# Kernel tuning notes

Hardware: AMD Instinct MI355X
Metric: run time of the kernel (lower is better)

Reference implementation:

```python
import jax, jax.numpy as jnp
import numpy as np

B, L, C, W, NH, FS = 8, 8, 64, 32, 128, 5
PAD = FS // 2
LN_EPS = 1e-5


def _conv(x, w, b, pad):
    y = jax.lax.conv_general_dilated(x, w, (1, 1), [(pad, pad), (pad, pad)],
                                     dimension_numbers=('NCHW', 'OIHW', 'NCHW'))
    return y + b[None, :, None, None]


def _stem(x, w1, b1, lnw, lnb, w2, b2):
    # conv(fs) -> LayerNorm over [C,W,W] -> ReLU -> conv(1x1)
    y = _conv(x, w1, b1, PAD)
    mu = jnp.mean(y, axis=(1, 2, 3), keepdims=True)
    var = jnp.var(y, axis=(1, 2, 3), keepdims=True)
    y = (y - mu) * jax.lax.rsqrt(var + LN_EPS) * lnw[None] + lnb[None]
    return _conv(jax.nn.relu(y), w2, b2, 0)


def setup_inputs() -> dict:
    key = jax.random.key(0)
    ks = jax.random.split(key, 8)
    f = lambda k, shp: jax.random.normal(k, shp, jnp.float32) * 0.02
    return {
        'in_query': jax.random.normal(ks[0], (B, C, W, W), jnp.float32),
        'in_keys': jax.random.normal(ks[1], (B, L, C, W, W), jnp.float32),
        'in_values': jax.random.normal(ks[2], (B, L, C, W, W), jnp.float32),
        's_w1': f(ks[3], (C, C, FS, FS)), 's_b1': jnp.zeros((C,), jnp.float32),
        's_lnw': jnp.ones((C, W, W), jnp.float32), 's_lnb': jnp.zeros((C, W, W), jnp.float32),
        's_w2': f(ks[4], (NH, C, 1, 1)), 's_b2': jnp.zeros((NH,), jnp.float32),
        'c_w1': f(ks[5], (C, C, FS, FS)), 'c_b1': jnp.zeros((C,), jnp.float32),
        'c_lnw': jnp.ones((C, W, W), jnp.float32), 'c_lnb': jnp.zeros((C, W, W), jnp.float32),
        'c_w2': f(ks[6], (NH, C, 1, 1)), 'c_b2': jnp.zeros((NH,), jnp.float32),
    }


def reference(in_query, in_keys, in_values,
              s_w1, s_b1, s_lnw, s_lnb, s_w2, s_b2,
              c_w1, c_b1, c_lnw, c_lnb, c_w2, c_b2):
    b, c, w, h = in_query.shape
    l = in_keys.shape[1]
    # ---- spatial attention: tokens = pixels, features = channels ----
    qf = in_query.reshape(b, c, w * h).transpose(0, 2, 1)            # [B, WH, C]
    kf = in_keys.transpose(0, 1, 3, 4, 2).reshape(b, l * w * h, c)   # [B, LWH, C]
    vf = in_values.transpose(0, 1, 3, 4, 2).reshape(b, l * w * h, c)
    a_sp = jax.nn.softmax(jnp.einsum('bnc,bmc->bnm', qf, kf), axis=-1)  # [B, WH, LWH]
    sp = jnp.einsum('bnm,bmc->bnc', a_sp, vf).reshape(b, w, h, c).transpose(0, 3, 1, 2)
    # ---- channel attention: tokens = channels, features = pixels ----
    qc = in_query.reshape(b, c, w * h)                               # [B, C, WH]
    kc = in_keys.reshape(b, l * c, h * w)                            # [B, LC, WH]
    vc = in_values.reshape(b, l * c, h * w)
    a_ch = jax.nn.softmax(jnp.einsum('bcn,bmn->bcm', qc, kc), axis=-1)  # [B, C, LC]
    ch = jnp.einsum('bcm,bmn->bcn', a_ch, vc).reshape(b, c, w, h)
    # ---- conv-LN-ReLU-conv stems on residual-added branches ----
    s_attn = _stem(sp + in_query, s_w1, s_b1, s_lnw, s_lnb, s_w2, s_b2)
    c_attn = _stem(ch + in_query, c_w1, c_b1, c_lnw, c_lnb, c_w2, c_b2)
    return (s_attn, c_attn)
```

## Files before the change

kernel.cpp:

```cpp
#include <hip/hip_runtime.h>


#define LOG2E 1.44269504088896340736f

typedef __attribute__((ext_vector_type(8))) short short8;
typedef __attribute__((ext_vector_type(4))) float f4;

#define MFMA16(a, b, c) __builtin_amdgcn_mfma_f32_16x16x32_bf16(a, b, c, 0, 0, 0)

__device__ __forceinline__ unsigned short f2bf(float f) {
  union { float f; unsigned u; } v; v.f = f;
  unsigned r = v.u + 0x7FFFu + ((v.u >> 16) & 1u);
  return (unsigned short)(r >> 16);
}
__device__ __forceinline__ unsigned short f2bf_rz(float f) {
  union { float f; unsigned u; } v; v.f = f;
  return (unsigned short)(v.u >> 16);
}
__device__ __forceinline__ float bf2f(unsigned short h) {
  union { unsigned u; float f; } v; v.u = ((unsigned)h) << 16;
  return v.f;
}
__device__ __forceinline__ float exp2fast(float x) {
#if __has_builtin(__builtin_amdgcn_exp2f)
  return __builtin_amdgcn_exp2f(x);
#else
  return exp2f(x);
#endif
}

#define O_STATS 0ul
#define O_W1T   256ul
#define O_W2B   409856ul
#define O_QT    442624ul
#define O_KSP   1491200ul
#define O_VT    9879808ul
#define O_VCT   18268416ul
#define O_NUM   26657024ul
#define O_DEN   35045632ul
#define O_SP    35307776ul
#define O_PCH   43696384ul
#define O_XS    44220672ul
#define O_XC    45269248ul
#define O_YT    46317824ul

__global__ __launch_bounds__(256) void k1_prep_chanS(
    const float* __restrict__ q, const float* __restrict__ keys,
    const float* __restrict__ values,
    const float* __restrict__ sw1, const float* __restrict__ sw2,
    const float* __restrict__ cw1, const float* __restrict__ cw2,
    char* __restrict__ ws)
{
  __shared__ float T[64][65];
  const int job = blockIdx.x, t = threadIdx.x;

  if (job < 2176) {
    unsigned short* VTp = (unsigned short*)(ws + O_VT);
    unsigned short* KSP = (unsigned short*)(ws + O_KSP);
    unsigned short* VCT = (unsigned short*)(ws + O_VCT);
    unsigned short* QT  = (unsigned short*)(ws + O_QT);
    int kind, mat;
    if (job < 1024)      { kind = 0; mat = job >> 4; }
    else if (job < 2048) { kind = 1; mat = (job - 1024) >> 4; }
    else                 { kind = 2; mat = (job - 2048) >> 4; }
    const int pt = job & 15, p0 = pt * 64;
    const float* src = (kind == 0 ? keys : kind == 1 ? values : q) + (size_t)mat * 65536;

    const int r0 = t >> 4, c4 = (t & 15) * 4;
#pragma unroll
    for (int pass = 0; pass < 4; ++pass) {
      const int r = pass * 16 + r0;
      float4 v = *(const float4*)(src + (size_t)r * 1024 + p0 + c4);
      float vv[4] = {v.x, v.y, v.z, v.w};
      T[r][c4] = vv[0]; T[r][c4 + 1] = vv[1]; T[r][c4 + 2] = vv[2]; T[r][c4 + 3] = vv[3];
      if (kind == 1) {
        int b = mat >> 3, l = mat & 7;
        size_t gi = ((size_t)b * 64 + r) * 8192 + l * 1024 + p0 + c4;
        ushort4 o; unsigned short* op = (unsigned short*)&o;
#pragma unroll
        for (int j = 0; j < 4; ++j) op[j] = f2bf(vv[j]);
        *(ushort4*)(VTp + gi) = o;
      }
    }
    __syncthreads();
#pragma unroll
    for (int pass = 0; pass < 2; ++pass) {
      const int p = pass * 32 + (t >> 3), cs = (t & 7) * 8;
      short8 o;
#pragma unroll
      for (int j = 0; j < 8; ++j) o[j] = (short)f2bf(T[cs + j][p]);
      if (kind == 0) {
        int b = mat >> 3, l = mat & 7;
        *(short8*)(KSP + ((size_t)b * 8192 + l * 1024 + p0 + p) * 64 + cs) = o;
      } else if (kind == 1) {
        int b = mat >> 3, l = mat & 7;
        *(short8*)(VCT + ((size_t)b * 1024 + p0 + p) * 512 + l * 64 + cs) = o;
      } else {
        *(short8*)(QT + ((size_t)mat * 1024 + p0 + p) * 64 + cs) = o;
      }
    }
    return;
  }

  if (job < 3040) {
    unsigned i = (job - 2176) * 256u + t;
    if (i < 204800u) {
      unsigned ci = i & 63u, co = (i >> 6) & 63u, tt = i >> 12;
      unsigned off = tt % 25u, st = tt / 25u;
      const float* w = st ? cw1 : sw1;
      ((unsigned short*)(ws + O_W1T))[i] = f2bf(w[(co * 64u + ci) * 25u + off]);
      return;
    }
    i -= 204800u;
    if (i < 16384u) {
      unsigned c = i & 63u, nh = (i >> 6) & 127u, st = i >> 13;
      const float* w = st ? cw2 : sw2;
      ((unsigned short*)(ws + O_W2B))[i] = f2bf(w[nh * 64u + c]);
    }
    return;
  }

  {
    float* Sp = (float*)(ws + O_SP);
    const int bid = job - 3040;
    const int b = bid >> 6, colT = (bid >> 3) & 7, kt = bid & 7;
    const int w = t >> 6, lane = t & 63;
    const int low4 = lane & 15, quad = lane >> 4;
    const int col0 = colT * 64 + w * 16;

    f4 acc[4];
#pragma unroll
    for (int m = 0; m < 4; ++m) acc[m] = (f4){0.f, 0.f, 0.f, 0.f};

#pragma unroll
    for (int kst = 0; kst < 4; ++kst) {
      const int k = kt * 128 + kst * 32 + quad * 8;
      const float* kp = keys + ((size_t)(b * 512 + col0 + low4)) * 1024 + k;
      float4 u0 = *(const float4*)kp;
      float4 u1 = *(const float4*)(kp + 4);
      float kv[8] = {u0.x, u0.y, u0.z, u0.w, u1.x, u1.y, u1.z, u1.w};
      short8 bh, bl;
#pragma unroll
      for (int j = 0; j < 8; ++j) {
        unsigned short hi = f2bf(kv[j]);
        bh[j] = (short)hi;
        bl[j] = (short)f2bf(kv[j] - bf2f(hi));
      }
#pragma unroll
      for (int m = 0; m < 4; ++m) {
        const float* qp = q + ((size_t)(b * 64 + m * 16 + low4)) * 1024 + k;
        float4 w0 = *(const float4*)qp;
        float4 w1 = *(const float4*)(qp + 4);
        float qv[8] = {w0.x, w0.y, w0.z, w0.w, w1.x, w1.y, w1.z, w1.w};
        short8 ah, al;
#pragma unroll
        for (int j = 0; j < 8; ++j) {
          float sv = qv[j] * LOG2E;
          unsigned short hi = f2bf(sv);
          ah[j] = (short)hi;
          al[j] = (short)f2bf(sv - bf2f(hi));
        }
        acc[m] = MFMA16(ah, bh, acc[m]);
        acc[m] = MFMA16(al, bh, acc[m]);
        acc[m] = MFMA16(ah, bl, acc[m]);
      }
    }
#pragma unroll
    for (int m = 0; m < 4; ++m)
#pragma unroll
      for (int r = 0; r < 4; ++r)
        Sp[(((size_t)kt * 8 + b) * 64 + m * 16 + quad * 4 + r) * 512 + col0 + low4] = acc[m][r];
  }
}

__global__ __launch_bounds__(256) void k2_spat_soft(char* __restrict__ ws)
{
  __shared__ __align__(16) unsigned short Kt[4096];
  __shared__ __align__(16) unsigned short Vt[4096];
  __shared__ __align__(16) unsigned short Plds[4][32][72];

  if (blockIdx.x < 512) {
    const unsigned short* QT = (const unsigned short*)(ws + O_QT);
    const unsigned short* KSP = (const unsigned short*)(ws + O_KSP);
    const unsigned short* VTg = (const unsigned short*)(ws + O_VT);
    unsigned short* NUM = (unsigned short*)(ws + O_NUM);
    float* DEN = (float*)(ws + O_DEN);

    const int b = blockIdx.x >> 6;
    const int qt = (blockIdx.x >> 3) & 7;
    const int s = blockIdx.x & 7;
    const int w = threadIdx.x >> 6, lane = threadIdx.x & 63;
    const int low4 = lane & 15, quad = lane >> 4;

    const unsigned short* KSPb = KSP + (size_t)b * 8192 * 64;
    const unsigned short* VTb = VTg + (size_t)b * 64 * 8192;
    const int qbase = qt * 128 + w * 32;

    short8 qa[2][2];
#pragma unroll
    for (int mi = 0; mi < 2; ++mi)
#pragma unroll
      for (int ks = 0; ks < 2; ++ks) {
        short8 qr = *(const short8*)(QT + ((size_t)(b * 1024 + qbase + mi * 16 + low4)) * 64 + ks * 32 + quad * 8);
        short8 qs;
#pragma unroll
        for (int j = 0; j < 8; ++j) qs[j] = (short)f2bf(bf2f((unsigned short)qr[j]) * LOG2E);
        qa[mi][ks] = qs;
      }

    f4 accO[2][4];
    float den[2][4];
#pragma unroll
    for (int mi = 0; mi < 2; ++mi)
#pragma unroll
      for (int n = 0; n < 4; ++n) {
        accO[mi][n] = (f4){0.f, 0.f, 0.f, 0.f};
        den[mi][n] = 0.f;
      }

    for (int it = 0; it < 16; ++it) {
      const int kv0 = s * 1024 + it * 64;
#pragma unroll
      for (int pass = 0; pass < 2; ++pass) {
        const int id = pass * 256 + threadIdx.x;
        const int n = id >> 7, ks = (id >> 6) & 1, L = (id >> 2) & 15, q = id & 3;
        *(short8*)(&Kt[id * 8]) =
            *(const short8*)(KSPb + (size_t)(kv0 + n * 16 + L) * 64 + ks * 32 + q * 8);
        *(short8*)(&Vt[id * 8]) =
            *(const short8*)(VTb + (size_t)(n * 16 + L) * 8192 + kv0 + ks * 32 + q * 8);
      }
      __syncthreads();

      f4 sS[2][4];
#pragma unroll
      for (int mi = 0; mi < 2; ++mi)
#pragma unroll
        for (int n = 0; n < 4; ++n) sS[mi][n] = (f4){0.f, 0.f, 0.f, 0.f};
#pragma unroll
      for (int ks = 0; ks < 2; ++ks)
#pragma unroll
        for (int n = 0; n < 4; ++n) {
          short8 kb = *(const short8*)(&Kt[((n * 2 + ks) * 64 + low4 * 4 + quad) * 8]);
          sS[0][n] = MFMA16(qa[0][ks], kb, sS[0][n]);
          sS[1][n] = MFMA16(qa[1][ks], kb, sS[1][n]);
        }
#pragma unroll
      for (int mi = 0; mi < 2; ++mi)
#pragma unroll
        for (int n = 0; n < 4; ++n)
#pragma unroll
          for (int r = 0; r < 4; ++r) {
            float e = exp2fast(sS[mi][n][r]);
            den[mi][r] += e;
            Plds[w][mi * 16 + quad * 4 + r][n * 16 + low4] = f2bf_rz(e);
          }
#pragma unroll
      for (int ks = 0; ks < 2; ++ks) {
        short8 pa0 = *(const short8*)&Plds[w][low4][ks * 32 + quad * 8];
        short8 pa1 = *(const short8*)&Plds[w][16 + low4][ks * 32 + quad * 8];
#pragma unroll
        for (int n2 = 0; n2 < 4; ++n2) {
          short8 vb = *(const short8*)(&Vt[((n2 * 2 + ks) * 64 + low4 * 4 + quad) * 8]);
          accO[0][n2] = MFMA16(pa0, vb, accO[0][n2]);
          accO[1][n2] = MFMA16(pa1, vb, accO[1][n2]);
        }
      }
      __syncthreads();
    }

#pragma unroll
    for (int mi = 0; mi < 2; ++mi)
#pragma unroll
      for (int r = 0; r < 4; ++r)
#pragma unroll
        for (int o = 1; o < 16; o <<= 1) den[mi][r] += __shfl_xor(den[mi][r], o, 64);

#pragma unroll
    for (int mi = 0; mi < 2; ++mi)
#pragma unroll
      for (int r = 0; r < 4; ++r) {
        const int row = qbase + mi * 16 + quad * 4 + r;
#pragma unroll
        for (int n2 = 0; n2 < 4; ++n2)
          NUM[(((size_t)(b * 1024 + row)) * 8 + s) * 64 + n2 * 16 + low4] = f2bf(accO[mi][n2][r]);
        if (low4 == 0) DEN[((size_t)(b * 1024 + row)) * 8 + s] = den[mi][r];
      }
    return;
  }

  {
    const float* Sp = (const float*)(ws + O_SP);
    unsigned short* P = (unsigned short*)(ws + O_PCH);
    const int bid = blockIdx.x - 512;
    const int b = bid >> 2, rt = bid & 3;
    const int row = rt * 16 + (threadIdx.x >> 4), tc = threadIdx.x & 15;

    float sv[32];
    float mx = -1e30f;
#pragma unroll
    for (int jj = 0; jj < 32; ++jj) {
      const int col = jj * 16 + tc;
      size_t base = ((size_t)b * 64 + row) * 512 + col;
      float v = 0.f;
#pragma unroll
      for (int kt = 0; kt < 8; ++kt) v += Sp[base + (size_t)kt * 262144];
      sv[jj] = v;
      mx = fmaxf(mx, v);
    }
#pragma unroll
    for (int o = 1; o < 16; o <<= 1) mx = fmaxf(mx, __shfl_xor(mx, o, 64));
    float sum = 0.f;
#pragma unroll
    for (int jj = 0; jj < 32; ++jj) {
      float e = exp2fast(sv[jj] - mx);
      sv[jj] = e;
      sum += e;
    }
#pragma unroll
    for (int o = 1; o < 16; o <<= 1) sum += __shfl_xor(sum, o, 64);
    const float rs = 1.0f / sum;
#pragma unroll
    for (int jj = 0; jj < 32; ++jj)
      P[((size_t)b * 64 + row) * 512 + jj * 16 + tc] = f2bf(sv[jj] * rs);
  }
}

__global__ __launch_bounds__(256) void k3_fin_chanB(char* __restrict__ ws)
{
  const unsigned short* QT = (const unsigned short*)(ws + O_QT);

  if (blockIdx.x < 256) {
    const unsigned short* NUM = (const unsigned short*)(ws + O_NUM);
    const float* DEN = (const float*)(ws + O_DEN);
    unsigned short* Xs = (unsigned short*)(ws + O_XS);

    const unsigned i = blockIdx.x * 256u + threadIdx.x;
    const int c0 = (i & 7) * 8;
    const unsigned row = i >> 3;

    float4 d0 = *(const float4*)(DEN + (size_t)row * 8);
    float4 d1 = *(const float4*)(DEN + (size_t)row * 8 + 4);
    float rd = 1.0f / (d0.x + d0.y + d0.z + d0.w + d1.x + d1.y + d1.z + d1.w);

    float n8[8] = {0, 0, 0, 0, 0, 0, 0, 0};
#pragma unroll
    for (int s = 0; s < 8; ++s) {
      short8 pv = *(const short8*)(NUM + ((size_t)row * 8 + s) * 64 + c0);
#pragma unroll
      for (int j = 0; j < 8; ++j) n8[j] += bf2f((unsigned short)pv[j]);
    }
    size_t ob = (size_t)row * 64 + c0;
    short8 qv = *(const short8*)(QT + ob);
    short8 o8;
#pragma unroll
    for (int j = 0; j < 8; ++j)
      o8[j] = (short)f2bf(n8[j] * rd + bf2f((unsigned short)qv[j]));
    *(short8*)(Xs + ob) = o8;
    return;
  }

  {
    const unsigned short* P = (const unsigned short*)(ws + O_PCH);
    const unsigned short* Vct = (const unsigned short*)(ws + O_VCT);
    unsigned short* Xc = (unsigned short*)(ws + O_XC);

    const int bid = blockIdx.x - 256;
    const int b = bid >> 4, pt = bid & 15;
    const int w = threadIdx.x >> 6, lane = threadIdx.x & 63;
    const int low4 = lane & 15, quad = lane >> 4;
    const int p = pt * 64 + w * 16 + low4;

    f4 acc[4];
#pragma unroll
    for (int m = 0; m < 4; ++m) acc[m] = (f4){0.f, 0.f, 0.f, 0.f};

    for (int ks = 0; ks < 16; ++ks) {
      short8 vb = *(const short8*)(Vct + ((size_t)(b * 1024 + p)) * 512 + ks * 32 + quad * 8);
#pragma unroll
      for (int m = 0; m < 4; ++m) {
        short8 a = *(const short8*)(P + ((size_t)(b * 64 + m * 16 + low4)) * 512 + ks * 32 + quad * 8);
        acc[m] = MFMA16(a, vb, acc[m]);
      }
    }
#pragma unroll
    for (int m = 0; m < 4; ++m)
#pragma unroll
      for (int r = 0; r < 4; ++r) {
        const int c = m * 16 + quad * 4 + r;
        size_t o = ((size_t)(b * 1024 + p)) * 64 + c;
        Xc[o] = f2bf(acc[m][r] + bf2f(QT[o]));
      }
  }
}

__global__ __launch_bounds__(256) void k4_conv5(char* __restrict__ ws,
                                                const float* __restrict__ sb1,
                                                const float* __restrict__ cb1)
{
  const int id = blockIdx.x;
  const int s = id >> 8, b = (id >> 5) & 7, pt = id & 31;
  const int w = threadIdx.x >> 6, lane = threadIdx.x & 63;
  const int low4 = lane & 15, quad = lane >> 4;
  const int wsub = w & 1, half = w >> 1;

  const unsigned short* X = (const unsigned short*)(ws + (s ? O_XC : O_XS));
  const unsigned short* W1t = (const unsigned short*)(ws + O_W1T);
  unsigned short* Yt = (unsigned short*)(ws + O_YT);
  float* stats = (float*)(ws + O_STATS);
  const float* b1p = s ? cb1 : sb1;

  __shared__ float Hbuf[2][16][65];
  __shared__ float red[2][2];

  const int p = pt * 32 + wsub * 16 + low4;
  const int y0 = p >> 5, x0 = p & 31;

  f4 acc[4];
#pragma unroll
  for (int m = 0; m < 4; ++m) acc[m] = (f4){0.f, 0.f, 0.f, 0.f};

  const int o0 = half ? 13 : 0, o1 = half ? 25 : 13;
  for (int off = o0; off < o1; ++off) {
    const int dy = off / 5 - 2, dx = off % 5 - 2;
    const int ys = y0 + dy, xs = x0 + dx;
    const bool valid = ((unsigned)ys < 32u) & ((unsigned)xs < 32u);
    const int psrc = valid ? (p + dy * 32 + dx) : p;
    const unsigned short* xp = X + ((size_t)(b * 1024 + psrc)) * 64;
    const unsigned short* wp = W1t + ((size_t)((s * 25 + off) * 64)) * 64;
#pragma unroll
    for (int ks = 0; ks < 2; ++ks) {
      short8 bv = *(const short8*)(xp + ks * 32 + quad * 8);
      if (!valid) bv = (short8)0;
#pragma unroll
      for (int m = 0; m < 4; ++m) {
        short8 av = *(const short8*)(wp + (m * 16 + low4) * 64 + ks * 32 + quad * 8);
        acc[m] = MFMA16(av, bv, acc[m]);
      }
    }
  }

  if (half) {
#pragma unroll
    for (int m = 0; m < 4; ++m)
#pragma unroll
      for (int r = 0; r < 4; ++r)
        Hbuf[wsub][low4][m * 16 + quad * 4 + r] = acc[m][r];
  }
  __syncthreads();
  if (!half) {
    float ls = 0.f, ls2 = 0.f;
#pragma unroll
    for (int m = 0; m < 4; ++m)
#pragma unroll
      for (int r = 0; r < 4; ++r) {
        const int co = m * 16 + quad * 4 + r;
        float y = acc[m][r] + Hbuf[wsub][low4][co] + b1p[co];
        Yt[((size_t)((s * 8 + b) * 1024 + p)) * 64 + co] = f2bf(y);
        ls += y; ls2 += y * y;
      }
#pragma unroll
    for (int o = 1; o < 64; o <<= 1) {
      ls += __shfl_xor(ls, o, 64);
      ls2 += __shfl_xor(ls2, o, 64);
    }
    if (lane == 0) { red[0][wsub] = ls; red[1][wsub] = ls2; }
  }
  __syncthreads();
  if (threadIdx.x == 0) {
    atomicAdd(&stats[(s * 8 + b) * 2 + 0], red[0][0] + red[0][1]);
    atomicAdd(&stats[(s * 8 + b) * 2 + 1], red[1][0] + red[1][1]);
  }
}

__global__ __launch_bounds__(256) void k5_final(char* __restrict__ ws,
                                                const float* __restrict__ slnw,
                                                const float* __restrict__ slnb,
                                                const float* __restrict__ clnw,
                                                const float* __restrict__ clnb,
                                                const float* __restrict__ sb2,
                                                const float* __restrict__ cb2,
                                                float* __restrict__ out)
{
  const int id = blockIdx.x;
  const int s = id >> 7, b = (id >> 4) & 7, pt = id & 15;
  const int w = threadIdx.x >> 6, lane = threadIdx.x & 63;
  const int low4 = lane & 15, quad = lane >> 4;
  const int p2 = pt * 64 + w * 16 + low4;

  const unsigned short* Yt = (const unsigned short*)(ws + O_YT);
  const unsigned short* W2b = (const unsigned short*)(ws + O_W2B);
  const float* stats = (const float*)(ws + O_STATS);
  const float* lw = s ? clnw : slnw;
  const float* lb = s ? clnb : slnb;
  const float* b2p = s ? cb2 : sb2;

  const float inv = 1.0f / 65536.0f;
  const float mu = stats[(s * 8 + b) * 2 + 0] * inv;
  const float ms = stats[(s * 8 + b) * 2 + 1] * inv;
  const float rsig = rsqrtf(ms - mu * mu + 1e-5f);

  f4 acc[8];
#pragma unroll
  for (int m = 0; m < 8; ++m) acc[m] = (f4){0.f, 0.f, 0.f, 0.f};

#pragma unroll
  for (int ks = 0; ks < 2; ++ks) {
    size_t yo = ((size_t)((s * 8 + b) * 1024 + p2)) * 64 + ks * 32 + quad * 8;
    short8 yv = *(const short8*)(Yt + yo);
    short8 zv;
#pragma unroll
    for (int j = 0; j < 8; ++j) {
      const int c = ks * 32 + quad * 8 + j;
      float z = (bf2f((unsigned short)yv[j]) - mu) * rsig * lw[c * 1024 + p2] + lb[c * 1024 + p2];
      zv[j] = (short)f2bf(fmaxf(z, 0.f));
    }
#pragma unroll
    for (int m = 0; m < 8; ++m) {
      short8 a = *(const short8*)(W2b + ((size_t)(s * 128 + m * 16 + low4)) * 64 + ks * 32 + quad * 8);
      acc[m] = MFMA16(a, zv, acc[m]);
    }
  }
#pragma unroll
  for (int m = 0; m < 8; ++m)
#pragma unroll
    for (int r = 0; r < 4; ++r) {
      const int nh = m * 16 + quad * 4 + r;
      out[((size_t)((s * 8 + b) * 128 + nh)) * 1024 + p2] = acc[m][r] + b2p[nh];
    }
}

extern "C" void kernel_launch(void* const* d_in, const int* in_sizes, int n_in,
                              void* d_out, int out_size, void* d_ws, size_t ws_size,
                              hipStream_t stream)
{
  const float* q    = (const float*)d_in[0];
  const float* keys = (const float*)d_in[1];
  const float* vals = (const float*)d_in[2];
  const float* sw1  = (const float*)d_in[3];
  const float* sb1  = (const float*)d_in[4];
  const float* slnw = (const float*)d_in[5];
  const float* slnb = (const float*)d_in[6];
  const float* sw2  = (const float*)d_in[7];
  const float* sb2  = (const float*)d_in[8];
  const float* cw1  = (const float*)d_in[9];
  const float* cb1  = (const float*)d_in[10];
  const float* clnw = (const float*)d_in[11];
  const float* clnb = (const float*)d_in[12];
  const float* cw2  = (const float*)d_in[13];
  const float* cb2  = (const float*)d_in[14];
  char* ws = (char*)d_ws;

  hipMemsetAsync(ws + O_STATS, 0, 256, stream);
  k1_prep_chanS<<<3552, 256, 0, stream>>>(q, keys, vals, sw1, sw2, cw1, cw2, ws);
  k2_spat_soft<<<544, 256, 0, stream>>>(ws);
  k3_fin_chanB<<<384, 256, 0, stream>>>(ws);
  k4_conv5<<<512, 256, 0, stream>>>(ws, sb1, cb1);
  k5_final<<<256, 256, 0, stream>>>(ws, slnw, slnb, clnw, clnb, sb2, cb2, (float*)d_out);
}
```

Baseline: 235.9 us.

## Double-buffer spatial attention via direct LDS loads and rebalance all kernels

The spatial softmax kernel now double-buffers K/V tiles using global_load_lds, processes 64 query rows per wave over a 16-way KV split, and computes the denominator with an MFMA against a ones vector. The LOG2E scaling is folded into the K transpose. The value transpose buffer is dropped, and the channel branch reads fp32 values directly. The conv kernel splits taps across 8 waves, the final kernel splits heads across waves, and the LayerNorm weights are pretransposed to bf16. Together these aim to overlap loads with compute and raise parallelism, at the cost of more partial sums, larger workspace traffic and bf16 rounding of the LN weights.

After: 232.2 us. About the same (-1.5%).

```diff
diff --git a/kernel.cpp b/kernel.cpp
--- a/kernel.cpp
+++ b/kernel.cpp
@@ -7,6 +7,10 @@
 typedef __attribute__((ext_vector_type(4))) float f4;
 
 #define MFMA16(a, b, c) __builtin_amdgcn_mfma_f32_16x16x32_bf16(a, b, c, 0, 0, 0)
+
+#define GLOAD_LDS16(gp, lp) __builtin_amdgcn_global_load_lds( \
+    (const __attribute__((address_space(1))) void*)(gp), \
+    (__attribute__((address_space(3))) void*)(lp), 16, 0, 0)
 
 __device__ __forceinline__ unsigned short f2bf(float f) {
   union { float f; unsigned u; } v; v.f = f;
@@ -32,78 +36,92 @@
 #define O_STATS 0ul
 #define O_W1T   256ul
 #define O_W2B   409856ul
-#define O_QT    442624ul
-#define O_KSP   1491200ul
-#define O_VT    9879808ul
-#define O_VCT   18268416ul
-#define O_NUM   26657024ul
-#define O_DEN   35045632ul
-#define O_SP    35307776ul
-#define O_PCH   43696384ul
-#define O_XS    44220672ul
-#define O_XC    45269248ul
-#define O_YT    46317824ul
+#define O_LNW   442624ul
+#define O_LNB   704768ul
+#define O_QT    966912ul
+#define O_KSP   2015488ul
+#define O_VT    10404096ul
+#define O_NUM   18792704ul
+#define O_DEN   35569920ul
+#define O_SP    36094208ul
+#define O_PCH   40288512ul
+#define O_XS    40812800ul
+#define O_XC    41861376ul
+#define O_YT    42909952ul
 
 __global__ __launch_bounds__(256) void k1_prep_chanS(
     const float* __restrict__ q, const float* __restrict__ keys,
     const float* __restrict__ values,
-    const float* __restrict__ sw1, const float* __restrict__ sw2,
-    const float* __restrict__ cw1, const float* __restrict__ cw2,
+    const float* __restrict__ sw1, const float* __restrict__ slnw,
+    const float* __restrict__ slnb, const float* __restrict__ sw2,
+    const float* __restrict__ cw1, const float* __restrict__ clnw,
+    const float* __restrict__ clnb, const float* __restrict__ cw2,
     char* __restrict__ ws)
 {
   __shared__ float T[64][65];
   const int job = blockIdx.x, t = threadIdx.x;
 
-  if (job < 2176) {
-    unsigned short* VTp = (unsigned short*)(ws + O_VT);
-    unsigned short* KSP = (unsigned short*)(ws + O_KSP);
-    unsigned short* VCT = (unsigned short*)(ws + O_VCT);
-    unsigned short* QT  = (unsigned short*)(ws + O_QT);
-    int kind, mat;
+  if (job < 2240) {
+    int kind, mat = 0, sel = 0;
     if (job < 1024)      { kind = 0; mat = job >> 4; }
     else if (job < 2048) { kind = 1; mat = (job - 1024) >> 4; }
-    else                 { kind = 2; mat = (job - 2048) >> 4; }
+    else if (job < 2176) { kind = 2; mat = (job - 2048) >> 4; }
+    else                 { kind = 3; sel = (job - 2176) >> 4; }
     const int pt = job & 15, p0 = pt * 64;
-    const float* src = (kind == 0 ? keys : kind == 1 ? values : q) + (size_t)mat * 65536;
+    const float* src =
+        kind == 0 ? keys : kind == 1 ? values : kind == 2 ? q
+        : (sel == 0 ? slnw : sel == 1 ? slnb : sel == 2 ? clnw : clnb);
+    src += (size_t)mat * 65536;
 
     const int r0 = t >> 4, c4 = (t & 15) * 4;
+    if (kind == 1) {
+      unsigned short* VTp = (unsigned short*)(ws + O_VT);
+      const int b = mat >> 3, l = mat & 7;
+#pragma unroll
+      for (int pass = 0; pass < 4; ++pass) {
+        const int r = pass * 16 + r0;
+        float4 v = *(const float4*)(src + (size_t)r * 1024 + p0 + c4);
+        ushort4 o;
+        o.x = f2bf(v.x); o.y = f2bf(v.y); o.z = f2bf(v.z); o.w = f2bf(v.w);
+        *(ushort4*)(VTp + ((size_t)b * 64 + r) * 8192 + l * 1024 + p0 + c4) = o;
+      }
+      return;
+    }
 #pragma unroll
     for (int pass = 0; pass < 4; ++pass) {
       const int r = pass * 16 + r0;
       float4 v = *(const float4*)(src + (size_t)r * 1024 + p0 + c4);
-      float vv[4] = {v.x, v.y, v.z, v.w};
-      T[r][c4] = vv[0]; T[r][c4 + 1] = vv[1]; T[r][c4 + 2] = vv[2]; T[r][c4 + 3] = vv[3];
-      if (kind == 1) {
-        int b = mat >> 3, l = mat & 7;
-        size_t gi = ((size_t)b * 64 + r) * 8192 + l * 1024 + p0 + c4;
-        ushort4 o; unsigned short* op = (unsigned short*)&o;
-#pragma unroll
-        for (int j = 0; j < 4; ++j) op[j] = f2bf(vv[j]);
-        *(ushort4*)(VTp + gi) = o;
-      }
+      T[r][c4] = v.x; T[r][c4 + 1] = v.y; T[r][c4 + 2] = v.z; T[r][c4 + 3] = v.w;
     }
     __syncthreads();
 #pragma unroll
     for (int pass = 0; pass < 2; ++pass) {
       const int p = pass * 32 + (t >> 3), cs = (t & 7) * 8;
       short8 o;
-#pragma unroll
-      for (int j = 0; j < 8; ++j) o[j] = (short)f2bf(T[cs + j][p]);
       if (kind == 0) {
-        int b = mat >> 3, l = mat & 7;
-        *(short8*)(KSP + ((size_t)b * 8192 + l * 1024 + p0 + p) * 64 + cs) = o;
-      } else if (kind == 1) {
-        int b = mat >> 3, l = mat & 7;
-        *(short8*)(VCT + ((size_t)b * 1024 + p0 + p) * 512 + l * 64 + cs) = o;
+#pragma unroll
+        for (int j = 0; j < 8; ++j) o[j] = (short)f2bf(T[cs + j][p] * LOG2E);
+        const int b = mat >> 3, l = mat & 7;
+        *(short8*)((unsigned short*)(ws + O_KSP) +
+                   ((size_t)b * 8192 + l * 1024 + p0 + p) * 64 + cs) = o;
+      } else if (kind == 2) {
+#pragma unroll
+        for (int j = 0; j < 8; ++j) o[j] = (short)f2bf(T[cs + j][p]);
+        *(short8*)((unsigned short*)(ws + O_QT) +
+                   ((size_t)mat * 1024 + p0 + p) * 64 + cs) = o;
       } else {
-        *(short8*)(QT + ((size_t)mat * 1024 + p0 + p) * 64 + cs) = o;
+#pragma unroll
+        for (int j = 0; j < 8; ++j) o[j] = (short)f2bf(T[cs + j][p]);
+        unsigned long off = (sel & 1) ? O_LNB : O_LNW;
+        *(short8*)((unsigned short*)(ws + off) +
+                   ((size_t)(sel >> 1) * 1024 + p0 + p) * 64 + cs) = o;
       }
     }
     return;
   }
 
-  if (job < 3040) {
-    unsigned i = (job - 2176) * 256u + t;
+  if (job < 3104) {
+    unsigned i = (job - 2240) * 256u + t;
     if (i < 204800u) {
       unsigned ci = i & 63u, co = (i >> 6) & 63u, tt = i >> 12;
       unsigned off = tt % 25u, st = tt / 25u;
@@ -122,8 +140,8 @@
 
   {
     float* Sp = (float*)(ws + O_SP);
-    const int bid = job - 3040;
-    const int b = bid >> 6, colT = (bid >> 3) & 7, kt = bid & 7;
+    const int bid = job - 3104;
+    const int b = bid >> 5, colT = (bid >> 2) & 7, kt = bid & 3;
     const int w = t >> 6, lane = t & 63;
     const int low4 = lane & 15, quad = lane >> 4;
     const int col0 = colT * 64 + w * 16;
@@ -133,8 +151,8 @@
     for (int m = 0; m < 4; ++m) acc[m] = (f4){0.f, 0.f, 0.f, 0.f};
 
 #pragma unroll
-    for (int kst = 0; kst < 4; ++kst) {
-      const int k = kt * 128 + kst * 32 + quad * 8;
+    for (int kst = 0; kst < 8; ++kst) {
+      const int k = kt * 256 + kst * 32 + quad * 8;
       const float* kp = keys + ((size_t)(b * 512 + col0 + low4)) * 1024 + k;
       float4 u0 = *(const float4*)kp;
       float4 u1 = *(const float4*)(kp + 4);
@@ -173,11 +191,11 @@
   }
 }
 
-__global__ __launch_bounds__(256) void k2_spat_soft(char* __restrict__ ws)
+__global__ __launch_bounds__(256, 2) void k2_spat_soft(char* __restrict__ ws)
 {
-  __shared__ __align__(16) unsigned short Kt[4096];
-  __shared__ __align__(16) unsigned short Vt[4096];
-  __shared__ __align__(16) unsigned short Plds[4][32][72];
+  __shared__ __align__(16) unsigned short Kt[2][4096];
+  __shared__ __align__(16) unsigned short Vt[2][4096];
+  __shared__ __align__(16) unsigned short Pl[4][4096];
 
   if (blockIdx.x < 512) {
     const unsigned short* QT = (const unsigned short*)(ws + O_QT);
@@ -187,103 +205,119 @@
     float* DEN = (float*)(ws + O_DEN);
 
     const int b = blockIdx.x >> 6;
-    const int qt = (blockIdx.x >> 3) & 7;
-    const int s = blockIdx.x & 7;
-    const int w = threadIdx.x >> 6, lane = threadIdx.x & 63;
+    const int qt = (blockIdx.x >> 4) & 3;
+    const int s = blockIdx.x & 15;
+    const int t = threadIdx.x;
+    const int w = t >> 6, lane = t & 63;
     const int low4 = lane & 15, quad = lane >> 4;
 
     const unsigned short* KSPb = KSP + (size_t)b * 8192 * 64;
     const unsigned short* VTb = VTg + (size_t)b * 64 * 8192;
-    const int qbase = qt * 128 + w * 32;
-
-    short8 qa[2][2];
-#pragma unroll
-    for (int mi = 0; mi < 2; ++mi)
+    const int qbase = qt * 256 + w * 64;
+    const int kvbase = s * 512;
+
+    int cn[2], cks[2], cqd[2], cl4[2];
+#pragma unroll
+    for (int pass = 0; pass < 2; ++pass) {
+      const int c = pass * 256 + t;
+      cn[pass] = c >> 7; cks[pass] = (c >> 6) & 1;
+      cqd[pass] = (c >> 4) & 3; cl4[pass] = c & 15;
+    }
+
+    short8 qa[4][2];
+#pragma unroll
+    for (int mi = 0; mi < 4; ++mi)
+#pragma unroll
+      for (int ks = 0; ks < 2; ++ks)
+        qa[mi][ks] = *(const short8*)(QT +
+            ((size_t)(b * 1024 + qbase + mi * 16 + low4)) * 64 + ks * 32 + quad * 8);
+
+    short8 vones;
+#pragma unroll
+    for (int j = 0; j < 8; ++j) vones[j] = (short)0x3F80;
+
+    f4 accO[4][4], accD[4];
+#pragma unroll
+    for (int m = 0; m < 4; ++m) {
+      accD[m] = (f4){0.f, 0.f, 0.f, 0.f};
+#pragma unroll
+      for (int n = 0; n < 4; ++n) accO[m][n] = (f4){0.f, 0.f, 0.f, 0.f};
+    }
+
+#pragma unroll
+    for (int pass = 0; pass < 2; ++pass) {
+      const int kv0 = kvbase;
+      GLOAD_LDS16(KSPb + ((size_t)(kv0 + cn[pass] * 16 + cl4[pass])) * 64 +
+                      cks[pass] * 32 + cqd[pass] * 8,
+                  &Kt[0][(pass * 256 + w * 64) * 8]);
+      GLOAD_LDS16(VTb + ((size_t)(cn[pass] * 16 + cl4[pass])) * 8192 + kv0 +
+                      cks[pass] * 32 + cqd[pass] * 8,
+                  &Vt[0][(pass * 256 + w * 64) * 8]);
+    }
+
+    const int pswz = ((low4 >> 2) & 3) << 1;
+    for (int it = 0; it < 8; ++it) {
+      const int d = it & 1;
+      __syncthreads();
+      if (it < 7) {
+        const int kv1 = kvbase + (it + 1) * 64;
+#pragma unroll
+        for (int pass = 0; pass < 2; ++pass) {
+          GLOAD_LDS16(KSPb + ((size_t)(kv1 + cn[pass] * 16 + cl4[pass])) * 64 +
+                          cks[pass] * 32 + cqd[pass] * 8,
+                      &Kt[d ^ 1][(pass * 256 + w * 64) * 8]);
+          GLOAD_LDS16(VTb + ((size_t)(cn[pass] * 16 + cl4[pass])) * 8192 + kv1 +
+                          cks[pass] * 32 + cqd[pass] * 8,
+                      &Vt[d ^ 1][(pass * 256 + w * 64) * 8]);
+        }
+      }
+#pragma unroll
+      for (int n = 0; n < 4; ++n) {
+        f4 sS[4];
+#pragma unroll
+        for (int mi = 0; mi < 4; ++mi) sS[mi] = (f4){0.f, 0.f, 0.f, 0.f};
+#pragma unroll
+        for (int ks = 0; ks < 2; ++ks) {
+          short8 kb = *(const short8*)&Kt[d][((n * 2 + ks) * 64 + lane) * 8];
+#pragma unroll
+          for (int mi = 0; mi < 4; ++mi) sS[mi] = MFMA16(qa[mi][ks], kb, sS[mi]);
+        }
+        const int cpr = (((n * 2 + (low4 >> 3)) ^ (quad << 1)) << 3) + (low4 & 7);
+#pragma unroll
+        for (int mi = 0; mi < 4; ++mi) {
+          unsigned short* pw = &Pl[w][(mi * 16 + quad * 4) * 64 + cpr];
+#pragma unroll
+          for (int r = 0; r < 4; ++r)
+            pw[r * 64] = f2bf_rz(exp2fast(sS[mi][r]));
+        }
+      }
 #pragma unroll
       for (int ks = 0; ks < 2; ++ks) {
-        short8 qr = *(const short8*)(QT + ((size_t)(b * 1024 + qbase + mi * 16 + low4)) * 64 + ks * 32 + quad * 8);
-        short8 qs;
-#pragma unroll
-        for (int j = 0; j < 8; ++j) qs[j] = (short)f2bf(bf2f((unsigned short)qr[j]) * LOG2E);
-        qa[mi][ks] = qs;
-      }
-
-    f4 accO[2][4];
-    float den[2][4];
-#pragma unroll
-    for (int mi = 0; mi < 2; ++mi)
-#pragma unroll
-      for (int n = 0; n < 4; ++n) {
-        accO[mi][n] = (f4){0.f, 0.f, 0.f, 0.f};
-        den[mi][n] = 0.f;
-      }
-
-    for (int it = 0; it < 16; ++it) {
-      const int kv0 = s * 1024 + it * 64;
-#pragma unroll
-      for (int pass = 0; pass < 2; ++pass) {
-        const int id = pass * 256 + threadIdx.x;
-        const int n = id >> 7, ks = (id >> 6) & 1, L = (id >> 2) & 15, q = id & 3;
-        *(short8*)(&Kt[id * 8]) =
-            *(const short8*)(KSPb + (size_t)(kv0 + n * 16 + L) * 64 + ks * 32 + q * 8);
-        *(short8*)(&Vt[id * 8]) =
-            *(const short8*)(VTb + (size_t)(n * 16 + L) * 8192 + kv0 + ks * 32 + q * 8);
-      }
-      __syncthreads();
-
-      f4 sS[2][4];
-#pragma unroll
-      for (int mi = 0; mi < 2; ++mi)
-#pragma unroll
-        for (int n = 0; n < 4; ++n) sS[mi][n] = (f4){0.f, 0.f, 0.f, 0.f};
-#pragma unroll
-      for (int ks = 0; ks < 2; ++ks)
-#pragma unroll
-        for (int n = 0; n < 4; ++n) {
-          short8 kb = *(const short8*)(&Kt[((n * 2 + ks) * 64 + low4 * 4 + quad) * 8]);
-          sS[0][n] = MFMA16(qa[0][ks], kb, sS[0][n]);
-          sS[1][n] = MFMA16(qa[1][ks], kb, sS[1][n]);
+        short8 vb[4];
+#pragma unroll
+        for (int n2 = 0; n2 < 4; ++n2)
+          vb[n2] = *(const short8*)&Vt[d][((n2 * 2 + ks) * 64 + lane) * 8];
+        const int cr = (((ks * 4 + quad) ^ pswz) << 3);
+#pragma unroll
+        for (int m = 0; m < 4; ++m) {
+          short8 pa = *(const short8*)&Pl[w][(m * 16 + low4) * 64 + cr];
+          accD[m] = MFMA16(pa, vones, accD[m]);
+#pragma unroll
+          for (int n2 = 0; n2 < 4; ++n2) accO[m][n2] = MFMA16(pa, vb[n2], accO[m][n2]);
         }
-#pragma unroll
-      for (int mi = 0; mi < 2; ++mi)
-#pragma unroll
-        for (int n = 0; n < 4; ++n)
-#pragma unroll
-          for (int r = 0; r < 4; ++r) {
-            float e = exp2fast(sS[mi][n][r]);
-            den[mi][r] += e;
-            Plds[w][mi * 16 + quad * 4 + r][n * 16 + low4] = f2bf_rz(e);
-          }
-#pragma unroll
-      for (int ks = 0; ks < 2; ++ks) {
-        short8 pa0 = *(const short8*)&Plds[w][low4][ks * 32 + quad * 8];
-        short8 pa1 = *(const short8*)&Plds[w][16 + low4][ks * 32 + quad * 8];
-#pragma unroll
-        for (int n2 = 0; n2 < 4; ++n2) {
-          short8 vb = *(const short8*)(&Vt[((n2 * 2 + ks) * 64 + low4 * 4 + quad) * 8]);
-          accO[0][n2] = MFMA16(pa0, vb, accO[0][n2]);
-          accO[1][n2] = MFMA16(pa1, vb, accO[1][n2]);
-        }
-      }
-      __syncthreads();
-    }
-
-#pragma unroll
-    for (int mi = 0; mi < 2; ++mi)
-#pragma unroll
-      for (int r = 0; r < 4; ++r)
-#pragma unroll
-        for (int o = 1; o < 16; o <<= 1) den[mi][r] += __shfl_xor(den[mi][r], o, 64);
-
-#pragma unroll
-    for (int mi = 0; mi < 2; ++mi)
+      }
+    }
+
+#pragma unroll
+    for (int m = 0; m < 4; ++m)
 #pragma unroll
       for (int r = 0; r < 4; ++r) {
-        const int row = qbase + mi * 16 + quad * 4 + r;
+        const int row = qbase + m * 16 + quad * 4 + r;
+        const size_t base = ((size_t)(b * 1024 + row) * 16 + s);
 #pragma unroll
         for (int n2 = 0; n2 < 4; ++n2)
-          NUM[(((size_t)(b * 1024 + row)) * 8 + s) * 64 + n2 * 16 + low4] = f2bf(accO[mi][n2][r]);
-        if (low4 == 0) DEN[((size_t)(b * 1024 + row)) * 8 + s] = den[mi][r];
+          NUM[base * 64 + n2 * 16 + low4] = f2bf(accO[m][n2][r]);
+        if (low4 == 0) DEN[base] = accD[m][r];
       }
     return;
   }
@@ -301,9 +335,7 @@
     for (int jj = 0; jj < 32; ++jj) {
       const int col = jj * 16 + tc;
       size_t base = ((size_t)b * 64 + row) * 512 + col;
-      float v = 0.f;
-#pragma unroll
-      for (int kt = 0; kt < 8; ++kt) v += Sp[base + (size_t)kt * 262144];
+      float v = Sp[base] + Sp[base + 262144] + Sp[base + 524288] + Sp[base + 786432];
       sv[jj] = v;
       mx = fmaxf(mx, v);
     }
@@ -325,46 +357,50 @@
   }
 }
 
-__global__ __launch_bounds__(256) void k3_fin_chanB(char* __restrict__ ws)
+__global__ __launch_bounds__(256) void k3_fin_chanB(const float* __restrict__ values,
+                                                    char* __restrict__ ws)
 {
   const unsigned short* QT = (const unsigned short*)(ws + O_QT);
 
-  if (blockIdx.x < 256) {
+  if (blockIdx.x < 512) {
     const unsigned short* NUM = (const unsigned short*)(ws + O_NUM);
     const float* DEN = (const float*)(ws + O_DEN);
     unsigned short* Xs = (unsigned short*)(ws + O_XS);
 
     const unsigned i = blockIdx.x * 256u + threadIdx.x;
-    const int c0 = (i & 7) * 8;
-    const unsigned row = i >> 3;
-
-    float4 d0 = *(const float4*)(DEN + (size_t)row * 8);
-    float4 d1 = *(const float4*)(DEN + (size_t)row * 8 + 4);
-    float rd = 1.0f / (d0.x + d0.y + d0.z + d0.w + d1.x + d1.y + d1.z + d1.w);
-
-    float n8[8] = {0, 0, 0, 0, 0, 0, 0, 0};
-#pragma unroll
-    for (int s = 0; s < 8; ++s) {
-      short8 pv = *(const short8*)(NUM + ((size_t)row * 8 + s) * 64 + c0);
-#pragma unroll
-      for (int j = 0; j < 8; ++j) n8[j] += bf2f((unsigned short)pv[j]);
-    }
+    const int c0 = (i & 15) * 4;
+    const unsigned row = i >> 4;
+
+    float dtot = 0.f;
+#pragma unroll
+    for (int sq = 0; sq < 4; ++sq) {
+      float4 dv = *(const float4*)(DEN + (size_t)row * 16 + sq * 4);
+      dtot += dv.x + dv.y + dv.z + dv.w;
+    }
+    float n4[4] = {0.f, 0.f, 0.f, 0.f};
+#pragma unroll
+    for (int s = 0; s < 16; ++s) {
+      ushort4 pv = *(const ushort4*)(NUM + ((size_t)row * 16 + s) * 64 + c0);
+      n4[0] += bf2f(pv.x); n4[1] += bf2f(pv.y);
+      n4[2] += bf2f(pv.z); n4[3] += bf2f(pv.w);
+    }
+    const float rd = 1.0f / dtot;
     size_t ob = (size_t)row * 64 + c0;
-    short8 qv = *(const short8*)(QT + ob);
-    short8 o8;
-#pragma unroll
-    for (int j = 0; j < 8; ++j)
-      o8[j] = (short)f2bf(n8[j] * rd + bf2f((unsigned short)qv[j]));
-    *(short8*)(Xs + ob) = o8;
+    ushort4 qv = *(const ushort4*)(QT + ob);
+    ushort4 o4;
+    o4.x = f2bf(n4[0] * rd + bf2f(qv.x));
+    o4.y = f2bf(n4[1] * rd + bf2f(qv.y));
+    o4.z = f2bf(n4[2] * rd + bf2f(qv.z));
+    o4.w = f2bf(n4[3] * rd + bf2f(qv.w));
+    *(ushort4*)(Xs + ob) = o4;
     return;
   }
 
   {
     const unsigned short* P = (const unsigned short*)(ws + O_PCH);
-    const unsigned short* Vct = (const unsigned short*)(ws + O_VCT);
     unsigned short* Xc = (unsigned short*)(ws + O_XC);
 
-    const int bid = blockIdx.x - 256;
+    const int bid = blockIdx.x - 512;
     const int b = bid >> 4, pt = bid & 15;
     const int w = threadIdx.x >> 6, lane = threadIdx.x & 63;
     const int low4 = lane & 15, quad = lane >> 4;
@@ -374,12 +410,16 @@
 #pragma unroll
     for (int m = 0; m < 4; ++m) acc[m] = (f4){0.f, 0.f, 0.f, 0.f};
 
+    const float* vbase = values + (size_t)b * 524288 + p;
     for (int ks = 0; ks < 16; ++ks) {
-      short8 vb = *(const short8*)(Vct + ((size_t)(b * 1024 + p)) * 512 + ks * 32 + quad * 8);
+      short8 vbv;
+      const float* vp = vbase + (size_t)(ks * 32 + quad * 8) * 1024;
+#pragma unroll
+      for (int j = 0; j < 8; ++j) vbv[j] = (short)f2bf(vp[(size_t)j * 1024]);
 #pragma unroll
       for (int m = 0; m < 4; ++m) {
         short8 a = *(const short8*)(P + ((size_t)(b * 64 + m * 16 + low4)) * 512 + ks * 32 + quad * 8);
-        acc[m] = MFMA16(a, vb, acc[m]);
+        acc[m] = MFMA16(a, vbv, acc[m]);
       }
     }
 #pragma unroll
@@ -393,15 +433,16 @@
   }
 }
 
-__global__ __launch_bounds__(256) void k4_conv5(char* __restrict__ ws,
+__global__ __launch_bounds__(512) void k4_conv5(char* __restrict__ ws,
                                                 const float* __restrict__ sb1,
                                                 const float* __restrict__ cb1)
 {
   const int id = blockIdx.x;
   const int s = id >> 8, b = (id >> 5) & 7, pt = id & 31;
-  const int w = threadIdx.x >> 6, lane = threadIdx.x & 63;
+  const int t = threadIdx.x;
+  const int w = t >> 6, lane = t & 63;
   const int low4 = lane & 15, quad = lane >> 4;
-  const int wsub = w & 1, half = w >> 1;
+  const int wsub = w & 1, quarter = w >> 1;
 
   const unsigned short* X = (const unsigned short*)(ws + (s ? O_XC : O_XS));
   const unsigned short* W1t = (const unsigned short*)(ws + O_W1T);
@@ -409,7 +450,7 @@
   float* stats = (float*)(ws + O_STATS);
   const float* b1p = s ? cb1 : sb1;
 
-  __shared__ float Hbuf[2][16][65];
+  __shared__ float Hbuf[3][2][16][65];
   __shared__ float red[2][2];
 
   const int p = pt * 32 + wsub * 16 + low4;
@@ -419,7 +460,8 @@
 #pragma unroll
   for (int m = 0; m < 4; ++m) acc[m] = (f4){0.f, 0.f, 0.f, 0.f};
 
-  const int o0 = half ? 13 : 0, o1 = half ? 25 : 13;
+  const int o0 = quarter == 0 ? 0 : quarter == 1 ? 7 : quarter == 2 ? 13 : 19;
+  const int o1 = quarter == 0 ? 7 : quarter == 1 ? 13 : quarter == 2 ? 19 : 25;
   for (int off = o0; off < o1; ++off) {
     const int dy = off / 5 - 2, dx = off % 5 - 2;
     const int ys = y0 + dy, xs = x0 + dx;
@@ -439,22 +481,23 @@
     }
   }
 
-  if (half) {
+  if (quarter) {
 #pragma unroll
     for (int m = 0; m < 4; ++m)
 #pragma unroll
       for (int r = 0; r < 4; ++r)
-        Hbuf[wsub][low4][m * 16 + quad * 4 + r] = acc[m][r];
+        Hbuf[quarter - 1][wsub][low4][m * 16 + quad * 4 + r] = acc[m][r];
   }
   __syncthreads();
-  if (!half) {
+  if (!quarter) {
     float ls = 0.f, ls2 = 0.f;
 #pragma unroll
     for (int m = 0; m < 4; ++m)
 #pragma unroll
       for (int r = 0; r < 4; ++r) {
         const int co = m * 16 + quad * 4 + r;
-        float y = acc[m][r] + Hbuf[wsub][low4][co] + b1p[co];
+        float y = acc[m][r] + Hbuf[0][wsub][low4][co] + Hbuf[1][wsub][low4][co] +
+                  Hbuf[2][wsub][low4][co] + b1p[co];
         Yt[((size_t)((s * 8 + b) * 1024 + p)) * 64 + co] = f2bf(y);
         ls += y; ls2 += y * y;
       }
@@ -466,32 +509,29 @@
     if (lane == 0) { red[0][wsub] = ls; red[1][wsub] = ls2; }
   }
   __syncthreads();
-  if (threadIdx.x == 0) {
+  if (t == 0) {
     atomicAdd(&stats[(s * 8 + b) * 2 + 0], red[0][0] + red[0][1]);
     atomicAdd(&stats[(s * 8 + b) * 2 + 1], red[1][0] + red[1][1]);
   }
 }
 
 __global__ __launch_bounds__(256) void k5_final(char* __restrict__ ws,
-                                                const float* __restrict__ slnw,
-                                                const float* __restrict__ slnb,
-                                                const float* __restrict__ clnw,
-                                                const float* __restrict__ clnb,
                                                 const float* __restrict__ sb2,
                                                 const float* __restrict__ cb2,
                                                 float* __restrict__ out)
 {
   const int id = blockIdx.x;
-  const int s = id >> 7, b = (id >> 4) & 7, pt = id & 15;
+  const int s = id >> 8, b = (id >> 5) & 7, pt = id & 31;
   const int w = threadIdx.x >> 6, lane = threadIdx.x & 63;
   const int low4 = lane & 15, quad = lane >> 4;
-  const int p2 = pt * 64 + w * 16 + low4;
+  const int p2 = pt * 32 + (w & 1) * 16 + low4;
+  const int nh0 = (w >> 1) * 64;
 
   const unsigned short* Yt = (const unsigned short*)(ws + O_YT);
+  const unsigned short* LNW = (const unsigned short*)(ws + O_LNW);
+  const unsigned short* LNB = (const unsigned short*)(ws + O_LNB);
   const unsigned short* W2b = (const unsigned short*)(ws + O_W2B);
   const float* stats = (const float*)(ws + O_STATS);
-  const float* lw = s ? clnw : slnw;
-  const float* lb = s ? clnb : slnb;
   const float* b2p = s ? cb2 : sb2;
 
   const float inv = 1.0f / 65536.0f;
@@ -499,32 +539,35 @@
   const float ms = stats[(s * 8 + b) * 2 + 1] * inv;
   const float rsig = rsqrtf(ms - mu * mu + 1e-5f);
 
-  f4 acc[8];
-#pragma unroll
-  for (int m = 0; m < 8; ++m) acc[m] = (f4){0.f, 0.f, 0.f, 0.f};
+  f4 acc[4];
+#pragma unroll
+  for (int m = 0; m < 4; ++m) acc[m] = (f4){0.f, 0.f, 0.f, 0.f};
 
 #pragma unroll
   for (int ks = 0; ks < 2; ++ks) {
     size_t yo = ((size_t)((s * 8 + b) * 1024 + p2)) * 64 + ks * 32 + quad * 8;
+    size_t lo = ((size_t)(s * 1024 + p2)) * 64 + ks * 32 + quad * 8;
     short8 yv = *(const short8*)(Yt + yo);
+    short8 lw8 = *(const short8*)(LNW + lo);
+    short8 lb8 = *(const short8*)(LNB + lo);
     short8 zv;
 #pragma unroll
     for (int j = 0; j < 8; ++j) {
-      const int c = ks * 32 + quad * 8 + j;
-      float z = (bf2f((unsigned short)yv[j]) - mu) * rsig * lw[c * 1024 + p2] + lb[c * 1024 + p2];
+      float z = (bf2f((unsigned short)yv[j]) - mu) * rsig * bf2f((unsigned short)lw8[j]) +
+                bf2f((unsigned short)lb8[j]);
       zv[j] = (short)f2bf(fmaxf(z, 0.f));
     }
 #pragma unroll
-    for (int m = 0; m < 8; ++m) {
-      short8 a = *(const short8*)(W2b + ((size_t)(s * 128 + m * 16 + low4)) * 64 + ks * 32 + quad * 8);
+    for (int m = 0; m < 4; ++m) {
+      short8 a = *(const short8*)(W2b + ((size_t)(s * 128 + nh0 + m * 16 + low4)) * 64 + ks * 32 + quad * 8);
       acc[m] = MFMA16(a, zv, acc[m]);
     }
   }
 #pragma unroll
-  for (int m = 0; m < 8; ++m)
+  for (int m = 0; m < 4; ++m)
 #pragma unroll
     for (int r = 0; r < 4; ++r) {
-      const int nh = m * 16 + quad * 4 + r;
+      const int nh = nh0 + m * 16 + quad * 4 + r;
       out[((size_t)((s * 8 + b) * 128 + nh)) * 1024 + p2] = acc[m][r] + b2p[nh];
     }
 }
@@ -551,9 +594,10 @@
   char* ws = (char*)d_ws;
 
   hipMemsetAsync(ws + O_STATS, 0, 256, stream);
-  k1_prep_chanS<<<3552, 256, 0, stream>>>(q, keys, vals, sw1, sw2, cw1, cw2, ws);
+  k1_prep_chanS<<<3360, 256, 0, stream>>>(q, keys, vals, sw1, slnw, slnb, sw2,
+                                          cw1, clnw, clnb, cw2, ws);
   k2_spat_soft<<<544, 256, 0, stream>>>(ws);
-  k3_fin_chanB<<<384, 256, 0, stream>>>(ws);
-  k4_conv5<<<512, 256, 0, stream>>>(ws, sb1, cb1);
-  k5_final<<<256, 256, 0, stream>>>(ws, slnw, slnb, clnw, clnb, sb2, cb2, (float*)d_out);
-}
+  k3_fin_chanB<<<640, 256, 0, stream>>>(vals, ws);
+  k4_conv5<<<512, 512, 0, stream>>>(ws, sb1, cb1);
+  k5_final<<<512, 256, 0, stream>>>(ws, sb2, cb2, (float*)d_out);
+}
```
